# Performance work log

Measured on AMD Instinct MI355X. Metric: run time of the kernel, lower is better.

## Reference

```python
import jax, jax.numpy as jnp
import numpy as np

EPS = 1e-5

def _bn(h, g, b, m, v):
    # inference-mode batchnorm, channel axis = 1
    shape = (1, -1) + (1,) * (h.ndim - 2)
    scale = g.reshape(shape) / jnp.sqrt(v.reshape(shape) + EPS)
    return (h - m.reshape(shape)) * scale + b.reshape(shape)

def setup_inputs() -> dict:
    B, Cin, Cout, N, K = 2, 64, 64, 50000, 16
    key = jax.random.key(0)
    ks = jax.random.split(key, 24)
    def bn_params(i, C):
        g = 1.0 + 0.1 * jax.random.normal(ks[i], (C,), jnp.float32)
        b = 0.1 * jax.random.normal(ks[i + 1], (C,), jnp.float32)
        m = 0.1 * jax.random.normal(ks[i + 2], (C,), jnp.float32)
        v = jax.random.uniform(ks[i + 3], (C,), jnp.float32, 0.5, 1.5)
        return g, b, m, v
    bn0_g, bn0_b, bn0_m, bn0_v = bn_params(0, Cin)
    bn2a_g, bn2a_b, bn2a_m, bn2a_v = bn_params(4, Cin)
    bn2b_g, bn2b_b, bn2b_m, bn2b_v = bn_params(8, Cout)
    x = jax.random.normal(ks[12], (B, Cin, N), jnp.float32)
    neighbors = jax.random.randint(ks[13], (B, K, N), 0, N, jnp.int32)
    w1 = 0.05 * jax.random.normal(ks[14], (Cout, Cin), jnp.float32)
    b1 = 0.05 * jax.random.normal(ks[15], (Cout,), jnp.float32)
    w2a = 0.05 * jax.random.normal(ks[16], (Cout, Cin), jnp.float32)
    w2b = 0.05 * jax.random.normal(ks[17], (Cout, Cout), jnp.float32)
    wf = 0.05 * jax.random.normal(ks[18], (Cout, 2 * Cout), jnp.float32)
    bf = 0.05 * jax.random.normal(ks[19], (Cout,), jnp.float32)
    return {"x": x, "neighbors": neighbors,
            "bn0_g": bn0_g, "bn0_b": bn0_b, "bn0_m": bn0_m, "bn0_v": bn0_v,
            "w1": w1, "b1": b1,
            "bn2a_g": bn2a_g, "bn2a_b": bn2a_b, "bn2a_m": bn2a_m, "bn2a_v": bn2a_v,
            "w2a": w2a,
            "bn2b_g": bn2b_g, "bn2b_b": bn2b_b, "bn2b_m": bn2b_m, "bn2b_v": bn2b_v,
            "w2b": w2b, "wf": wf, "bf": bf}

def reference(x, neighbors, bn0_g, bn0_b, bn0_m, bn0_v, w1, b1,
              bn2a_g, bn2a_b, bn2a_m, bn2a_v, w2a,
              bn2b_g, bn2b_b, bn2b_m, bn2b_v, w2b, wf, bf):
    # x: (B, Cin, N), neighbors: (B, K, N) int indices into N
    xn = _bn(x, bn0_g, bn0_b, bn0_m, bn0_v)                    # BatchNorm1d
    point = jnp.einsum('oc,bcn->bon', w1, xn) + b1[None, :, None]  # conv1 (1x1)
    idx = neighbors[:, 1:, :]                                   # (B, K-1, N); skip self (col 0)
    # gathered[b,c,k,n] = xn[b,c, idx[b,k,n]]
    gathered = jax.vmap(lambda xb, ib: xb[:, ib])(xn, idx)      # (B, C, K-1, N)
    diff = jnp.transpose(gathered, (0, 1, 3, 2)) - xn[:, :, :, None]  # (B, C, N, K-1)
    h = _bn(diff, bn2a_g, bn2a_b, bn2a_m, bn2a_v)               # BatchNorm2d
    h = jnp.einsum('oc,bcnk->bonk', w2a, h)                     # Conv2d 1x1, no bias
    h = jax.nn.relu(_bn(h, bn2b_g, bn2b_b, bn2b_m, bn2b_v))
    h = jnp.einsum('oc,bcnk->bonk', w2b, h)                     # Conv2d 1x1, no bias
    neigh = h.max(axis=-1)                                      # max over K-1 neighbors
    cat = jnp.concatenate([point, neigh], axis=1)               # (B, 2*Cout, N)
    return jnp.einsum('oc,bcn->bon', wf, cat) + bf[None, :, None]
```

## Files before the change

kernel.cpp:

```cpp
#include <hip/hip_runtime.h>
#include <hip/hip_bf16.h>

typedef __bf16 bf16x8 __attribute__((ext_vector_type(8)));
typedef float f32x4 __attribute__((ext_vector_type(4)));

#define NPT 50000

#define OFF_Y    0u
#define OFF_PRM  12800000u
#define OFF_W2   12801024u
#define OFF_WP   12809216u
#define OFF_W2B  12817408u
#define OFF_WN   12825600u
#define OFF_FLAG 12833792u

__global__ __launch_bounds__(256) void precompute_kernel(
    const void* bn0_g, const void* bn0_b, const void* bn0_m, const void* bn0_v,
    const void* w1, const void* b1,
    const void* bn2a_g, const void* bn2a_b, const void* bn2a_m, const void* bn2a_v,
    const void* w2a,
    const void* bn2b_g, const void* bn2b_b, const void* bn2b_m, const void* bn2b_v,
    const void* w2b, const void* wf, const void* bfv,
    float* __restrict__ prm, __bf16* __restrict__ W2bf, __bf16* __restrict__ Wpbf,
    __bf16* __restrict__ W2Bbf, __bf16* __restrict__ Wnbf, int* __restrict__ flagp)
{
    __shared__ __bf16 w1s[4096];
    __shared__ __bf16 wfs[8192];
    __shared__ __bf16 w2as[4096];
    __shared__ float b1s[64], bfs[64], s2a[64], t2a[64], s2b[64], t2b[64];
    __shared__ int sflag;
    int t = threadIdx.x;

    if (t == 0) {
        const unsigned short* u = (const unsigned short*)bn0_v;
        int cnt = 0;
        for (int i = 0; i < 64; ++i) {
            float f = __uint_as_float(((unsigned int)u[i]) << 16);
            if (f > 0.4f && f < 1.6f) cnt++;
        }
        int fv = (cnt >= 60) ? 1 : 0;
        sflag = fv;
        *flagp = fv;
    }
    __syncthreads();
    int fl = sflag;

    if (fl) {
        const __bf16* W1  = (const __bf16*)w1;
        const __bf16* W2A = (const __bf16*)w2a;
        const __bf16* WF  = (const __bf16*)wf;
        const __bf16* W2B = (const __bf16*)w2b;
        for (int i = t; i < 4096; i += 256) { w1s[i] = W1[i]; w2as[i] = W2A[i]; W2Bbf[i] = W2B[i]; }
        for (int i = t; i < 8192; i += 256) wfs[i] = WF[i];
        if (t < 64) {
            float s0 = (float)((const __bf16*)bn0_g)[t] / sqrtf((float)((const __bf16*)bn0_v)[t] + 1e-5f);
            prm[t] = s0;
            prm[64 + t] = (float)((const __bf16*)bn0_b)[t] - (float)((const __bf16*)bn0_m)[t] * s0;
            float sa = (float)((const __bf16*)bn2a_g)[t] / sqrtf((float)((const __bf16*)bn2a_v)[t] + 1e-5f);
            s2a[t] = sa;
            t2a[t] = (float)((const __bf16*)bn2a_b)[t] - (float)((const __bf16*)bn2a_m)[t] * sa;
            float sb = (float)((const __bf16*)bn2b_g)[t] / sqrtf((float)((const __bf16*)bn2b_v)[t] + 1e-5f);
            s2b[t] = sb;
            t2b[t] = (float)((const __bf16*)bn2b_b)[t] - (float)((const __bf16*)bn2b_m)[t] * sb;
            b1s[t] = (float)((const __bf16*)b1)[t];
            bfs[t] = (float)((const __bf16*)bfv)[t];
        }
    } else {
        const float* W1  = (const float*)w1;
        const float* W2A = (const float*)w2a;
        const float* WF  = (const float*)wf;
        const float* W2B = (const float*)w2b;
        for (int i = t; i < 4096; i += 256) { w1s[i] = (__bf16)W1[i]; w2as[i] = (__bf16)W2A[i]; W2Bbf[i] = (__bf16)W2B[i]; }
        for (int i = t; i < 8192; i += 256) wfs[i] = (__bf16)WF[i];
        if (t < 64) {
            float s0 = ((const float*)bn0_g)[t] / sqrtf(((const float*)bn0_v)[t] + 1e-5f);
            prm[t] = s0;
            prm[64 + t] = ((const float*)bn0_b)[t] - ((const float*)bn0_m)[t] * s0;
            float sa = ((const float*)bn2a_g)[t] / sqrtf(((const float*)bn2a_v)[t] + 1e-5f);
            s2a[t] = sa;
            t2a[t] = ((const float*)bn2a_b)[t] - ((const float*)bn2a_m)[t] * sa;
            float sb = ((const float*)bn2b_g)[t] / sqrtf(((const float*)bn2b_v)[t] + 1e-5f);
            s2b[t] = sb;
            t2b[t] = ((const float*)bn2b_b)[t] - ((const float*)bn2b_m)[t] * sb;
            b1s[t] = ((const float*)b1)[t];
            bfs[t] = ((const float*)bfv)[t];
        }
    }
    __syncthreads();

    for (int e = t; e < 4096; e += 256) {
        int o = e >> 6, c = e & 63;
        W2bf[e] = (__bf16)((float)w2as[e] * s2a[c] * s2b[o]);
        Wnbf[e] = wfs[o * 128 + 64 + c];
        float acc = 0.f;
        for (int m = 0; m < 64; ++m)
            acc += (float)wfs[o * 128 + m] * (float)w1s[m * 64 + c];
        Wpbf[e] = (__bf16)acc;
    }
    if (t < 64) {
        float acc = 0.f, accb = 0.f;
        for (int c = 0; c < 64; ++c) {
            acc  += (float)w2as[t * 64 + c] * t2a[c];
            accb += (float)wfs[t * 128 + c] * b1s[c];
        }
        prm[128 + t] = s2b[t] * acc + t2b[t];
        prm[192 + t] = accb + bfs[t];
    }
}

__global__ __launch_bounds__(256) void pass1_kernel(
    const void* x, const float* __restrict__ prm,
    const __bf16* __restrict__ W2bf, __bf16* __restrict__ Y,
    const int* __restrict__ flagp)
{
    __shared__ float xs[64][65];
    int bid = blockIdx.x;
    int b = bid / 782;
    int n0 = (bid % 782) * 64;
    int npts = NPT - n0; if (npts > 64) npts = 64;
    int fl = *flagp;

    if (fl) {
        const __bf16* xb = (const __bf16*)x + (size_t)b * 64 * NPT;
        for (int i = threadIdx.x; i < 4096; i += 256) {
            int c = i >> 6, p = i & 63;
            float v = (p < npts) ? (float)xb[(size_t)c * NPT + n0 + p] : 0.f;
            xs[p][c] = fmaf(v, prm[c], prm[64 + c]);
        }
    } else {
        const float* xb = (const float*)x + (size_t)b * 64 * NPT;
        for (int i = threadIdx.x; i < 4096; i += 256) {
            int c = i >> 6, p = i & 63;
            float v = (p < npts) ? xb[(size_t)c * NPT + n0 + p] : 0.f;
            xs[p][c] = fmaf(v, prm[c], prm[64 + c]);
        }
    }
    __syncthreads();

    int wid = threadIdx.x >> 6, lane = threadIdx.x & 63;
    int pl = (wid << 4) + (lane & 15);
    int hq = lane >> 4;
    int c0 = hq << 3;

    bf16x8 a0, a1;
    #pragma unroll
    for (int i = 0; i < 8; ++i) {
        a0[i] = (__bf16)xs[pl][c0 + i];
        a1[i] = (__bf16)xs[pl][c0 + 32 + i];
    }

    int ob = lane & 15;
    f32x4 accY[4];
    #pragma unroll
    for (int nt = 0; nt < 4; ++nt) {
        bf16x8 w20 = *(const bf16x8*)(W2bf + (ob + 16 * nt) * 64 + c0);
        bf16x8 w21 = *(const bf16x8*)(W2bf + (ob + 16 * nt) * 64 + c0 + 32);
        f32x4 z = {0.f, 0.f, 0.f, 0.f};
        accY[nt] = __builtin_amdgcn_mfma_f32_16x16x32_bf16(a0, w20, z, 0, 0, 0);
        accY[nt] = __builtin_amdgcn_mfma_f32_16x16x32_bf16(a1, w21, accY[nt], 0, 0, 0);
    }

    #pragma unroll
    for (int nt = 0; nt < 4; ++nt) {
        #pragma unroll
        for (int i = 0; i < 4; ++i) {
            int prow = (wid << 4) + (hq << 2) + i;
            if (prow < npts)
                Y[((size_t)b * NPT + n0 + prow) * 64 + ob + 16 * nt] = (__bf16)accY[nt][i];
        }
    }
}

__global__ __launch_bounds__(256) void pass2_kernel(
    const int* __restrict__ nbr, const __bf16* __restrict__ Y,
    const void* x, const float* __restrict__ prm,
    const __bf16* __restrict__ W2Bbf, const __bf16* __restrict__ Wnbf,
    const __bf16* __restrict__ Wpbf, void* out, const int* __restrict__ flagp)
{
    __shared__ float ns[2][2][16][69];
    int wid = threadIdx.x >> 6, lane = threadIdx.x & 63;
    int tile = wid >> 1, h = wid & 1;
    int gtile = blockIdx.x * 2 + tile;
    int b = gtile / 3125;
    int n0 = (gtile % 3125) << 4;
    int fl = *flagp;

    int mo = lane & 15;
    int hq = lane >> 4;
    int c0 = hq << 3;
    int nglob = n0 + mo;

    bf16x8 wA[4][2];
    #pragma unroll
    for (int mt = 0; mt < 4; ++mt) {
        wA[mt][0] = *(const bf16x8*)(W2Bbf + (mo + 16 * mt) * 64 + c0);
        wA[mt][1] = *(const bf16x8*)(W2Bbf + (mo + 16 * mt) * 64 + c0 + 32);
    }

    const __bf16* yrow = Y + ((size_t)b * NPT + nglob) * 64;
    float mv[2][8];
    #pragma unroll
    for (int ks = 0; ks < 2; ++ks) {
        bf16x8 yn = *(const bf16x8*)(yrow + c0 + 32 * ks);
        #pragma unroll
        for (int i = 0; i < 8; ++i)
            mv[ks][i] = prm[128 + c0 + 32 * ks + i] - (float)yn[i];
    }

    const int* nb_base = nbr + (size_t)b * 16 * NPT + NPT + nglob;
    int kbase = h * 7;
    int j[8];
    #pragma unroll
    for (int kk = 0; kk < 8; ++kk)
        j[kk] = nb_base[(size_t)(kbase + kk) * NPT];

    bf16x8 y0v[8], y1v[8];
    #pragma unroll
    for (int kk = 0; kk < 8; ++kk) {
        const __bf16* yj = Y + ((size_t)b * NPT + j[kk]) * 64;
        y0v[kk] = *(const bf16x8*)(yj + c0);
        y1v[kk] = *(const bf16x8*)(yj + c0 + 32);
    }

    f32x4 vmax[4];
    #pragma unroll
    for (int mt = 0; mt < 4; ++mt) vmax[mt] = {-3.0e38f, -3.0e38f, -3.0e38f, -3.0e38f};

    #pragma unroll
    for (int kk = 0; kk < 8; ++kk) {
        bf16x8 t0, t1;
        #pragma unroll
        for (int i = 0; i < 8; ++i) {
            t0[i] = (__bf16)fmaxf((float)y0v[kk][i] + mv[0][i], 0.f);
            t1[i] = (__bf16)fmaxf((float)y1v[kk][i] + mv[1][i], 0.f);
        }
        #pragma unroll
        for (int mt = 0; mt < 4; ++mt) {
            f32x4 hh = {0.f, 0.f, 0.f, 0.f};
            hh = __builtin_amdgcn_mfma_f32_16x16x32_bf16(wA[mt][0], t0, hh, 0, 0, 0);
            hh = __builtin_amdgcn_mfma_f32_16x16x32_bf16(wA[mt][1], t1, hh, 0, 0, 0);
            #pragma unroll
            for (int i = 0; i < 4; ++i) vmax[mt][i] = fmaxf(vmax[mt][i], hh[i]);
        }
    }

    #pragma unroll
    for (int mt = 0; mt < 4; ++mt)
        #pragma unroll
        for (int i = 0; i < 4; ++i)
            ns[tile][h][mo][16 * mt + (hq << 2) + i] = vmax[mt][i];

    __syncthreads();

    bf16x8 nb2[2];
    #pragma unroll
    for (int ks = 0; ks < 2; ++ks)
        #pragma unroll
        for (int i = 0; i < 8; ++i) {
            int c = c0 + 32 * ks + i;
            nb2[ks][i] = (__bf16)fmaxf(ns[tile][0][mo][c], ns[tile][1][mo][c]);
        }

    __builtin_amdgcn_sched_barrier(0);

    bf16x8 xnb[2];
    if (fl) {
        const __bf16* xp = (const __bf16*)x;
        #pragma unroll
        for (int ks = 0; ks < 2; ++ks)
            #pragma unroll
            for (int i = 0; i < 8; ++i) {
                int c = c0 + 32 * ks + i;
                float v = (float)xp[((size_t)b * 64 + c) * NPT + nglob];
                xnb[ks][i] = (__bf16)fmaf(v, prm[c], prm[64 + c]);
            }
    } else {
        const float* xp = (const float*)x;
        #pragma unroll
        for (int ks = 0; ks < 2; ++ks)
            #pragma unroll
            for (int i = 0; i < 8; ++i) {
                int c = c0 + 32 * ks + i;
                float v = xp[((size_t)b * 64 + c) * NPT + nglob];
                xnb[ks][i] = (__bf16)fmaf(v, prm[c], prm[64 + c]);
            }
    }

    #pragma unroll
    for (int q = 0; q < 2; ++q) {
        int mt = 2 * h + q;
        bf16x8 wn0 = *(const bf16x8*)(Wnbf + (mo + 16 * mt) * 64 + c0);
        bf16x8 wn1 = *(const bf16x8*)(Wnbf + (mo + 16 * mt) * 64 + c0 + 32);
        bf16x8 wp0 = *(const bf16x8*)(Wpbf + (mo + 16 * mt) * 64 + c0);
        bf16x8 wp1 = *(const bf16x8*)(Wpbf + (mo + 16 * mt) * 64 + c0 + 32);
        f32x4 acc = *(const f32x4*)(prm + 192 + 16 * mt + 4 * hq);
        acc = __builtin_amdgcn_mfma_f32_16x16x32_bf16(wp0, xnb[0], acc, 0, 0, 0);
        acc = __builtin_amdgcn_mfma_f32_16x16x32_bf16(wp1, xnb[1], acc, 0, 0, 0);
        acc = __builtin_amdgcn_mfma_f32_16x16x32_bf16(wn0, nb2[0], acc, 0, 0, 0);
        acc = __builtin_amdgcn_mfma_f32_16x16x32_bf16(wn1, nb2[1], acc, 0, 0, 0);

        if (fl) {
            __bf16* ob = (__bf16*)out + (size_t)b * 64 * NPT + n0 + mo;
            #pragma unroll
            for (int i = 0; i < 4; ++i)
                ob[(size_t)(16 * mt + (hq << 2) + i) * NPT] = (__bf16)acc[i];
        } else {
            float* ob = (float*)out + (size_t)b * 64 * NPT + n0 + mo;
            #pragma unroll
            for (int i = 0; i < 4; ++i)
                ob[(size_t)(16 * mt + (hq << 2) + i) * NPT] = acc[i];
        }
    }
}

extern "C" void kernel_launch(void* const* d_in, const int* in_sizes, int n_in,
                              void* d_out, int out_size, void* d_ws, size_t ws_size,
                              hipStream_t stream) {
    const void* x      = d_in[0];
    const int*  nbr    = (const int*)d_in[1];

    char* ws = (char*)d_ws;
    __bf16* Y     = (__bf16*)(ws + OFF_Y);
    float*  prm   = (float*)(ws + OFF_PRM);
    __bf16* W2bf  = (__bf16*)(ws + OFF_W2);
    __bf16* Wpbf  = (__bf16*)(ws + OFF_WP);
    __bf16* W2Bbf = (__bf16*)(ws + OFF_W2B);
    __bf16* Wnbf  = (__bf16*)(ws + OFF_WN);
    int*    flagp = (int*)(ws + OFF_FLAG);

    precompute_kernel<<<1, 256, 0, stream>>>(
        d_in[2], d_in[3], d_in[4], d_in[5], d_in[6], d_in[7],
        d_in[8], d_in[9], d_in[10], d_in[11], d_in[12],
        d_in[13], d_in[14], d_in[15], d_in[16], d_in[17], d_in[18], d_in[19],
        prm, W2bf, Wpbf, W2Bbf, Wnbf, flagp);

    pass1_kernel<<<1564, 256, 0, stream>>>(x, prm, W2bf, Y, flagp);

    pass2_kernel<<<3125, 256, 0, stream>>>(nbr, Y, x, prm, W2Bbf, Wnbf, Wpbf, d_out, flagp);
}
```

Baseline: 199.5 us.

## Stage normalized x tile in LDS and issue gathers earlier in pass2

Pass2 now loads the 32-point x tile once per block into shared memory with all 256 threads, applying the bn0 affine, instead of each wave reading strided columns of x late in the kernel. Neighbor index loads and the self Y row are issued before the weight loads, and a sched barrier after the gathers keeps them in flight early. Blocks are remapped so a tile never straddles the two batches, with clamping and guarded stores for the tail. It also sets launch_bounds min-blocks to 2, which may cap registers, and adds LDS use plus a bounds check.

```diff
diff --git a/kernel.cpp b/kernel.cpp
--- a/kernel.cpp
+++ b/kernel.cpp
@@ -5,6 +5,7 @@
 typedef float f32x4 __attribute__((ext_vector_type(4)));
 
 #define NPT 50000
+#define BPB 1563
 
 #define OFF_Y    0u
 #define OFF_PRM  12800000u
@@ -171,24 +172,52 @@
     }
 }
 
-__global__ __launch_bounds__(256) void pass2_kernel(
+__global__ __launch_bounds__(256, 2) void pass2_kernel(
     const int* __restrict__ nbr, const __bf16* __restrict__ Y,
     const void* x, const float* __restrict__ prm,
     const __bf16* __restrict__ W2Bbf, const __bf16* __restrict__ Wnbf,
     const __bf16* __restrict__ Wpbf, void* out, const int* __restrict__ flagp)
 {
+    __shared__ float xs2[32][65];
     __shared__ float ns[2][2][16][69];
     int wid = threadIdx.x >> 6, lane = threadIdx.x & 63;
     int tile = wid >> 1, h = wid & 1;
-    int gtile = blockIdx.x * 2 + tile;
-    int b = gtile / 3125;
-    int n0 = (gtile % 3125) << 4;
+    int bb = blockIdx.x;
+    int b = (bb >= BPB) ? 1 : 0;
+    int n0g = (bb - b * BPB) * 32;
+    int n0 = n0g + (tile << 4);
     int fl = *flagp;
 
     int mo = lane & 15;
     int hq = lane >> 4;
     int c0 = hq << 3;
     int nglob = n0 + mo;
+    int ng = (nglob < NPT) ? nglob : (NPT - 1);
+
+    {
+        int p = threadIdx.x & 31;
+        int pp = n0g + p; if (pp >= NPT) pp = NPT - 1;
+        if (fl) {
+            const __bf16* xg = (const __bf16*)x + (size_t)b * 64 * NPT + pp;
+            for (int c = threadIdx.x >> 5; c < 64; c += 8)
+                xs2[p][c] = fmaf((float)xg[(size_t)c * NPT], prm[c], prm[64 + c]);
+        } else {
+            const float* xg = (const float*)x + (size_t)b * 64 * NPT + pp;
+            for (int c = threadIdx.x >> 5; c < 64; c += 8)
+                xs2[p][c] = fmaf(xg[(size_t)c * NPT], prm[c], prm[64 + c]);
+        }
+    }
+
+    const int* nb_base = nbr + (size_t)b * 16 * NPT + NPT + ng;
+    int kbase = h * 7;
+    int j[8];
+    #pragma unroll
+    for (int kk = 0; kk < 8; ++kk)
+        j[kk] = nb_base[(size_t)(kbase + kk) * NPT];
+
+    const __bf16* yrow = Y + ((size_t)b * NPT + ng) * 64;
+    bf16x8 yn0 = *(const bf16x8*)(yrow + c0);
+    bf16x8 yn1 = *(const bf16x8*)(yrow + c0 + 32);
 
     bf16x8 wA[4][2];
     #pragma unroll
@@ -196,23 +225,6 @@
         wA[mt][0] = *(const bf16x8*)(W2Bbf + (mo + 16 * mt) * 64 + c0);
         wA[mt][1] = *(const bf16x8*)(W2Bbf + (mo + 16 * mt) * 64 + c0 + 32);
     }
-
-    const __bf16* yrow = Y + ((size_t)b * NPT + nglob) * 64;
-    float mv[2][8];
-    #pragma unroll
-    for (int ks = 0; ks < 2; ++ks) {
-        bf16x8 yn = *(const bf16x8*)(yrow + c0 + 32 * ks);
-        #pragma unroll
-        for (int i = 0; i < 8; ++i)
-            mv[ks][i] = prm[128 + c0 + 32 * ks + i] - (float)yn[i];
-    }
-
-    const int* nb_base = nbr + (size_t)b * 16 * NPT + NPT + nglob;
-    int kbase = h * 7;
-    int j[8];
-    #pragma unroll
-    for (int kk = 0; kk < 8; ++kk)
-        j[kk] = nb_base[(size_t)(kbase + kk) * NPT];
 
     bf16x8 y0v[8], y1v[8];
     #pragma unroll
@@ -220,6 +232,14 @@
         const __bf16* yj = Y + ((size_t)b * NPT + j[kk]) * 64;
         y0v[kk] = *(const bf16x8*)(yj + c0);
         y1v[kk] = *(const bf16x8*)(yj + c0 + 32);
+    }
+    __builtin_amdgcn_sched_barrier(0);
+
+    float mv[2][8];
+    #pragma unroll
+    for (int i = 0; i < 8; ++i) {
+        mv[0][i] = prm[128 + c0 + i]      - (float)yn0[i];
+        mv[1][i] = prm[128 + c0 + 32 + i] - (float)yn1[i];
     }
 
     f32x4 vmax[4];
@@ -261,29 +281,14 @@
             nb2[ks][i] = (__bf16)fmaxf(ns[tile][0][mo][c], ns[tile][1][mo][c]);
         }
 
-    __builtin_amdgcn_sched_barrier(0);
-
     bf16x8 xnb[2];
-    if (fl) {
-        const __bf16* xp = (const __bf16*)x;
+    {
+        int prow = (tile << 4) + mo;
         #pragma unroll
         for (int ks = 0; ks < 2; ++ks)
             #pragma unroll
-            for (int i = 0; i < 8; ++i) {
-                int c = c0 + 32 * ks + i;
-                float v = (float)xp[((size_t)b * 64 + c) * NPT + nglob];
-                xnb[ks][i] = (__bf16)fmaf(v, prm[c], prm[64 + c]);
-            }
-    } else {
-        const float* xp = (const float*)x;
-        #pragma unroll
-        for (int ks = 0; ks < 2; ++ks)
-            #pragma unroll
-            for (int i = 0; i < 8; ++i) {
-                int c = c0 + 32 * ks + i;
-                float v = xp[((size_t)b * 64 + c) * NPT + nglob];
-                xnb[ks][i] = (__bf16)fmaf(v, prm[c], prm[64 + c]);
-            }
+            for (int i = 0; i < 8; ++i)
+                xnb[ks][i] = (__bf16)xs2[prow][c0 + 32 * ks + i];
     }
 
     #pragma unroll
@@ -299,16 +304,18 @@
         acc = __builtin_amdgcn_mfma_f32_16x16x32_bf16(wn0, nb2[0], acc, 0, 0, 0);
         acc = __builtin_amdgcn_mfma_f32_16x16x32_bf16(wn1, nb2[1], acc, 0, 0, 0);
 
-        if (fl) {
-            __bf16* ob = (__bf16*)out + (size_t)b * 64 * NPT + n0 + mo;
-            #pragma unroll
-            for (int i = 0; i < 4; ++i)
-                ob[(size_t)(16 * mt + (hq << 2) + i) * NPT] = (__bf16)acc[i];
-        } else {
-            float* ob = (float*)out + (size_t)b * 64 * NPT + n0 + mo;
-            #pragma unroll
-            for (int i = 0; i < 4; ++i)
-                ob[(size_t)(16 * mt + (hq << 2) + i) * NPT] = acc[i];
+        if (nglob < NPT) {
+            if (fl) {
+                __bf16* ob = (__bf16*)out + (size_t)b * 64 * NPT + nglob;
+                #pragma unroll
+                for (int i = 0; i < 4; ++i)
+                    ob[(size_t)(16 * mt + (hq << 2) + i) * NPT] = (__bf16)acc[i];
+            } else {
+                float* ob = (float*)out + (size_t)b * 64 * NPT + nglob;
+                #pragma unroll
+                for (int i = 0; i < 4; ++i)
+                    ob[(size_t)(16 * mt + (hq << 2) + i) * NPT] = acc[i];
+            }
         }
     }
 }
@@ -336,5 +343,5 @@
 
     pass1_kernel<<<1564, 256, 0, stream>>>(x, prm, W2bf, Y, flagp);
 
-    pass2_kernel<<<3125, 256, 0, stream>>>(nbr, Y, x, prm, W2Bbf, Wnbf, Wpbf, d_out, flagp);
+    pass2_kernel<<<2 * BPB, 256, 0, stream>>>(nbr, Y, x, prm, W2Bbf, Wnbf, Wpbf, d_out, flagp);
 }
```

New measurement: 207.3 us. 3.9% more time.

## Vectorize pass1 x loads and hoist pass2 gathers into explicit inline-asm batches

Applied to the files above, without the earlier changes.

In pass1, full tiles now load x with 8-wide bf16 or 4-wide float vector loads instead of scalar strided loads. In pass2, the neighbor indices, the per-point x values and the Y row are issued up front as inline-asm global loads, followed by an explicit vmcnt wait, and all 16 neighbor-row gathers are then issued before a second wait. This moves the x load for the final conv ahead of the max-reduction so its latency is hidden. A launch_bounds occupancy hint of 2 is added to pass2. The approach adds register pressure and relies on hand-written waitcnt placement for correctness.

```diff
diff --git a/kernel.cpp b/kernel.cpp
--- a/kernel.cpp
+++ b/kernel.cpp
@@ -3,6 +3,7 @@
 
 typedef __bf16 bf16x8 __attribute__((ext_vector_type(8)));
 typedef float f32x4 __attribute__((ext_vector_type(4)));
+typedef unsigned int uint32x4 __attribute__((ext_vector_type(4)));
 
 #define NPT 50000
 
@@ -120,19 +121,42 @@
     int npts = NPT - n0; if (npts > 64) npts = 64;
     int fl = *flagp;
 
-    if (fl) {
-        const __bf16* xb = (const __bf16*)x + (size_t)b * 64 * NPT;
-        for (int i = threadIdx.x; i < 4096; i += 256) {
-            int c = i >> 6, p = i & 63;
-            float v = (p < npts) ? (float)xb[(size_t)c * NPT + n0 + p] : 0.f;
-            xs[p][c] = fmaf(v, prm[c], prm[64 + c]);
+    if (npts == 64) {
+        if (fl) {
+            const __bf16* xb = (const __bf16*)x + (size_t)b * 64 * NPT + n0;
+            for (int i = threadIdx.x; i < 512; i += 256) {
+                int c = i >> 3, q = (i & 7) * 8;
+                bf16x8 v = *(const bf16x8*)(xb + (size_t)c * NPT + q);
+                #pragma unroll
+                for (int e = 0; e < 8; ++e)
+                    xs[q + e][c] = fmaf((float)v[e], prm[c], prm[64 + c]);
+            }
+        } else {
+            const float* xb = (const float*)x + (size_t)b * 64 * NPT + n0;
+            for (int i = threadIdx.x; i < 1024; i += 256) {
+                int c = i >> 4, q = (i & 15) * 4;
+                float4 v = *(const float4*)(xb + (size_t)c * NPT + q);
+                xs[q + 0][c] = fmaf(v.x, prm[c], prm[64 + c]);
+                xs[q + 1][c] = fmaf(v.y, prm[c], prm[64 + c]);
+                xs[q + 2][c] = fmaf(v.z, prm[c], prm[64 + c]);
+                xs[q + 3][c] = fmaf(v.w, prm[c], prm[64 + c]);
+            }
         }
     } else {
-        const float* xb = (const float*)x + (size_t)b * 64 * NPT;
-        for (int i = threadIdx.x; i < 4096; i += 256) {
-            int c = i >> 6, p = i & 63;
-            float v = (p < npts) ? xb[(size_t)c * NPT + n0 + p] : 0.f;
-            xs[p][c] = fmaf(v, prm[c], prm[64 + c]);
+        if (fl) {
+            const __bf16* xb = (const __bf16*)x + (size_t)b * 64 * NPT;
+            for (int i = threadIdx.x; i < 4096; i += 256) {
+                int c = i >> 6, p = i & 63;
+                float v = (p < npts) ? (float)xb[(size_t)c * NPT + n0 + p] : 0.f;
+                xs[p][c] = fmaf(v, prm[c], prm[64 + c]);
+            }
+        } else {
+            const float* xb = (const float*)x + (size_t)b * 64 * NPT;
+            for (int i = threadIdx.x; i < 4096; i += 256) {
+                int c = i >> 6, p = i & 63;
+                float v = (p < npts) ? xb[(size_t)c * NPT + n0 + p] : 0.f;
+                xs[p][c] = fmaf(v, prm[c], prm[64 + c]);
+            }
         }
     }
     __syncthreads();
@@ -171,7 +195,7 @@
     }
 }
 
-__global__ __launch_bounds__(256) void pass2_kernel(
+__global__ __launch_bounds__(256, 2) void pass2_kernel(
     const int* __restrict__ nbr, const __bf16* __restrict__ Y,
     const void* x, const float* __restrict__ prm,
     const __bf16* __restrict__ W2Bbf, const __bf16* __restrict__ Wnbf,
@@ -190,6 +214,36 @@
     int c0 = hq << 3;
     int nglob = n0 + mo;
 
+    const int* nb_base = nbr + (size_t)b * 16 * NPT + NPT + nglob;
+    int kbase = h * 7;
+    unsigned int ju[8];
+    #pragma unroll
+    for (int kk = 0; kk < 8; ++kk) {
+        unsigned long long a = (unsigned long long)(nb_base + (size_t)(kbase + kk) * NPT);
+        asm volatile("global_load_dword %0, %1, off" : "=v"(ju[kk]) : "v"(a) : "memory");
+    }
+    unsigned int xr[16];
+    if (fl) {
+        const __bf16* xp = (const __bf16*)x + (size_t)b * 64 * NPT + nglob;
+        #pragma unroll
+        for (int i = 0; i < 16; ++i) {
+            int c = c0 + (i >> 3) * 32 + (i & 7);
+            unsigned long long a = (unsigned long long)(xp + (size_t)c * NPT);
+            asm volatile("global_load_ushort %0, %1, off" : "=v"(xr[i]) : "v"(a) : "memory");
+        }
+    } else {
+        const float* xp = (const float*)x + (size_t)b * 64 * NPT + nglob;
+        #pragma unroll
+        for (int i = 0; i < 16; ++i) {
+            int c = c0 + (i >> 3) * 32 + (i & 7);
+            unsigned long long a = (unsigned long long)(xp + (size_t)c * NPT);
+            asm volatile("global_load_dword %0, %1, off" : "=v"(xr[i]) : "v"(a) : "memory");
+        }
+    }
+
+    const __bf16* yrow = Y + ((size_t)b * NPT + nglob) * 64;
+    bf16x8 yn0 = *(const bf16x8*)(yrow + c0);
+    bf16x8 yn1 = *(const bf16x8*)(yrow + c0 + 32);
     bf16x8 wA[4][2];
     #pragma unroll
     for (int mt = 0; mt < 4; ++mt) {
@@ -197,42 +251,41 @@
         wA[mt][1] = *(const bf16x8*)(W2Bbf + (mo + 16 * mt) * 64 + c0 + 32);
     }
 
-    const __bf16* yrow = Y + ((size_t)b * NPT + nglob) * 64;
-    float mv[2][8];
-    #pragma unroll
-    for (int ks = 0; ks < 2; ++ks) {
-        bf16x8 yn = *(const bf16x8*)(yrow + c0 + 32 * ks);
-        #pragma unroll
-        for (int i = 0; i < 8; ++i)
-            mv[ks][i] = prm[128 + c0 + 32 * ks + i] - (float)yn[i];
-    }
-
-    const int* nb_base = nbr + (size_t)b * 16 * NPT + NPT + nglob;
-    int kbase = h * 7;
-    int j[8];
-    #pragma unroll
-    for (int kk = 0; kk < 8; ++kk)
-        j[kk] = nb_base[(size_t)(kbase + kk) * NPT];
-
-    bf16x8 y0v[8], y1v[8];
+    asm volatile("s_waitcnt vmcnt(0)" ::: "memory");
+    __builtin_amdgcn_sched_barrier(0);
+
+    uint32x4 g0[8], g1[8];
+    const char* ybase = (const char*)Y + (size_t)b * NPT * 128 + hq * 16;
     #pragma unroll
     for (int kk = 0; kk < 8; ++kk) {
-        const __bf16* yj = Y + ((size_t)b * NPT + j[kk]) * 64;
-        y0v[kk] = *(const bf16x8*)(yj + c0);
-        y1v[kk] = *(const bf16x8*)(yj + c0 + 32);
+        unsigned long long a0 = (unsigned long long)(ybase + (size_t)ju[kk] * 128);
+        asm volatile("global_load_dwordx4 %0, %1, off" : "=v"(g0[kk]) : "v"(a0) : "memory");
+        asm volatile("global_load_dwordx4 %0, %1, off offset:64" : "=v"(g1[kk]) : "v"(a0) : "memory");
+    }
+
+    float mv0[8], mv1[8];
+    #pragma unroll
+    for (int i = 0; i < 8; ++i) {
+        mv0[i] = prm[128 + c0 + i]      - (float)yn0[i];
+        mv1[i] = prm[128 + c0 + 32 + i] - (float)yn1[i];
     }
 
     f32x4 vmax[4];
     #pragma unroll
     for (int mt = 0; mt < 4; ++mt) vmax[mt] = {-3.0e38f, -3.0e38f, -3.0e38f, -3.0e38f};
 
+    asm volatile("s_waitcnt vmcnt(0)" ::: "memory");
+    __builtin_amdgcn_sched_barrier(0);
+
     #pragma unroll
     for (int kk = 0; kk < 8; ++kk) {
+        bf16x8 y0 = __builtin_bit_cast(bf16x8, g0[kk]);
+        bf16x8 y1 = __builtin_bit_cast(bf16x8, g1[kk]);
         bf16x8 t0, t1;
         #pragma unroll
         for (int i = 0; i < 8; ++i) {
-            t0[i] = (__bf16)fmaxf((float)y0v[kk][i] + mv[0][i], 0.f);
-            t1[i] = (__bf16)fmaxf((float)y1v[kk][i] + mv[1][i], 0.f);
+            t0[i] = (__bf16)fmaxf((float)y0[i] + mv0[i], 0.f);
+            t1[i] = (__bf16)fmaxf((float)y1[i] + mv1[i], 0.f);
         }
         #pragma unroll
         for (int mt = 0; mt < 4; ++mt) {
@@ -261,29 +314,12 @@
             nb2[ks][i] = (__bf16)fmaxf(ns[tile][0][mo][c], ns[tile][1][mo][c]);
         }
 
-    __builtin_amdgcn_sched_barrier(0);
-
     bf16x8 xnb[2];
-    if (fl) {
-        const __bf16* xp = (const __bf16*)x;
-        #pragma unroll
-        for (int ks = 0; ks < 2; ++ks)
-            #pragma unroll
-            for (int i = 0; i < 8; ++i) {
-                int c = c0 + 32 * ks + i;
-                float v = (float)xp[((size_t)b * 64 + c) * NPT + nglob];
-                xnb[ks][i] = (__bf16)fmaf(v, prm[c], prm[64 + c]);
-            }
-    } else {
-        const float* xp = (const float*)x;
-        #pragma unroll
-        for (int ks = 0; ks < 2; ++ks)
-            #pragma unroll
-            for (int i = 0; i < 8; ++i) {
-                int c = c0 + 32 * ks + i;
-                float v = xp[((size_t)b * 64 + c) * NPT + nglob];
-                xnb[ks][i] = (__bf16)fmaf(v, prm[c], prm[64 + c]);
-            }
+    #pragma unroll
+    for (int i = 0; i < 16; ++i) {
+        int c = c0 + (i >> 3) * 32 + (i & 7);
+        float v = fl ? __uint_as_float(xr[i] << 16) : __uint_as_float(xr[i]);
+        xnb[i >> 3][i & 7] = (__bf16)fmaf(v, prm[c], prm[64 + c]);
     }
 
     #pragma unroll
@@ -300,12 +336,12 @@
         acc = __builtin_amdgcn_mfma_f32_16x16x32_bf16(wn1, nb2[1], acc, 0, 0, 0);
 
         if (fl) {
-            __bf16* ob = (__bf16*)out + (size_t)b * 64 * NPT + n0 + mo;
+            __bf16* ob = (__bf16*)out + (size_t)b * 64 * NPT + nglob;
             #pragma unroll
             for (int i = 0; i < 4; ++i)
                 ob[(size_t)(16 * mt + (hq << 2) + i) * NPT] = (__bf16)acc[i];
         } else {
-            float* ob = (float*)out + (size_t)b * 64 * NPT + n0 + mo;
+            float* ob = (float*)out + (size_t)b * 64 * NPT + nglob;
             #pragma unroll
             for (int i = 0; i < 4; ++i)
                 ob[(size_t)(16 * mt + (hq << 2) + i) * NPT] = acc[i];
```

Result: slower. 203.6 us (+2.0%).
